# Kernel optimization log

Measured on AMD Instinct MI355X. Metric: run time of the kernel, lower is better.

Reference implementation:

```python
import jax, jax.numpy as jnp
import numpy as np

N_NODES = 100000
N_EDGES = 600000
C_IN, C_HID, C_OUT = 256, 128, 128
LN_EPS = 1e-5
NEG_SLOPE = 0.01  # nn.LeakyReLU default


def setup_inputs() -> dict:
    key = jax.random.key(0)
    ks = jax.random.split(key, 9)
    x = jax.random.normal(ks[0], (N_NODES, C_IN), dtype=jnp.float32)
    x_struct = jax.random.normal(ks[1], (1,), dtype=jnp.float32)  # unused by forward
    x_e = jax.random.normal(ks[2], (1,), dtype=jnp.float32)       # unused by forward
    edge_index = jax.random.randint(ks[3], (2, N_EDGES), 0, N_NODES, dtype=jnp.int64)
    W1 = jax.random.normal(ks[4], (C_IN, C_HID), dtype=jnp.float32) / np.sqrt(C_IN)
    b1 = jnp.zeros((C_HID,), dtype=jnp.float32)
    gamma = jnp.ones((C_HID,), dtype=jnp.float32)
    beta = jnp.zeros((C_HID,), dtype=jnp.float32)
    W2 = jax.random.normal(ks[5], (C_HID, C_OUT), dtype=jnp.float32) / np.sqrt(C_HID)
    b2 = jnp.zeros((C_OUT,), dtype=jnp.float32)
    return {"x": x, "x_struct": x_struct, "x_e": x_e, "edge_index": edge_index,
            "W1": W1, "b1": b1, "gamma": gamma, "beta": beta, "W2": W2, "b2": b2}


def reference(x, x_struct, x_e, edge_index, W1, b1, gamma, beta, W2, b2):
    # dropout is identity in eval mode
    h = jax.nn.leaky_relu(x @ W1 + b1, negative_slope=NEG_SLOPE)  # [N, H]
    # LayerNorm over last dim
    mu = jnp.mean(h, axis=-1, keepdims=True)
    var = jnp.mean(jnp.square(h - mu), axis=-1, keepdims=True)
    h = (h - mu) * jax.lax.rsqrt(var + LN_EPS) * gamma + beta
    # gather source-node features, scatter-min into destination nodes
    src, dst = edge_index[0], edge_index[1]
    msgs = h[src]                                                 # [E, H]
    agg = jax.ops.segment_min(msgs, dst, num_segments=N_NODES)   # empty -> +inf
    counts = jax.ops.segment_sum(jnp.ones((msgs.shape[0],), dtype=jnp.float32),
                                 dst, num_segments=N_NODES)
    agg = jnp.where(counts[:, None] > 0, agg, 0.0)               # PyG fills empty with 0
    return agg @ W2 + b2                                          # [N, C_OUT]
```

## Files before the change

kernel.cpp:

```cpp
#include <hip/hip_runtime.h>
#include <hip/hip_bf16.h>
#include <cstdint>

#define N_NODES 100000
#define N_EDGES 600000
#define C_IN    256
#define C_HID   128
#define C_OUT   128
#define LN_EPS  1e-5f
#define NEG_SLOPE 0.01f

#define NSCAN_BLOCKS 391

typedef float f32x4 __attribute__((ext_vector_type(4)));
typedef __attribute__((ext_vector_type(8))) short frag_ab;

__device__ __forceinline__ void split2(float f, ushort& h, ushort& l) {
    unsigned u = __float_as_uint(f);
    h = (ushort)(u >> 16);
    float d = f - __uint_as_float(u & 0xFFFF0000u);
    l = (ushort)(__float_as_uint(d) >> 16);
}

__device__ __forceinline__ void split8(const float4& p, const float4& q,
                                       frag_ab& hi, frag_ab& lo) {
    ushort h, l;
    split2(p.x, h, l); hi[0] = (short)h; lo[0] = (short)l;
    split2(p.y, h, l); hi[1] = (short)h; lo[1] = (short)l;
    split2(p.z, h, l); hi[2] = (short)h; lo[2] = (short)l;
    split2(p.w, h, l); hi[3] = (short)h; lo[3] = (short)l;
    split2(q.x, h, l); hi[4] = (short)h; lo[4] = (short)l;
    split2(q.y, h, l); hi[5] = (short)h; lo[5] = (short)l;
    split2(q.z, h, l); hi[6] = (short)h; lo[6] = (short)l;
    split2(q.w, h, l); hi[7] = (short)h; lo[7] = (short)l;
}

__device__ __forceinline__ void gload_lds16(const void* g, void* l) {
    __builtin_amdgcn_global_load_lds(
        (const __attribute__((address_space(1))) unsigned int*)g,
        (__attribute__((address_space(3))) unsigned int*)l, 16, 0, 0);
}

__global__ __launch_bounds__(256) void setup_kernel(
    const float* __restrict__ W1, const float* __restrict__ W2,
    ushort* __restrict__ w1s, ushort* __restrict__ w2s, int* __restrict__ dz)
{
    int tg = blockIdx.x * 256 + threadIdx.x;
    if (tg < 2 * N_NODES) dz[tg] = 0;

    const float* W; ushort* out; int t;
    if (tg < 4096)      { W = W1; out = w1s; t = tg; }
    else if (tg < 6144) { W = W2; out = w2s; t = tg - 4096; }
    else return;

    int lane = t & 63;
    int ks   = (t >> 6) & 3;
    int nf   = (t >> 8) & 7;
    int kc   = t >> 11;
    int k0   = kc * 128 + ks * 32 + (lane >> 4) * 8;
    int n    = nf * 16 + (lane & 15);

    frag_ab hi, lo;
    #pragma unroll
    for (int j = 0; j < 8; ++j) {
        ushort h, l;
        split2(W[(size_t)(k0 + j) * 128 + n], h, l);
        hi[j] = (short)h; lo[j] = (short)l;
    }
    size_t fi = ((size_t)(kc * 4 + ks) * 16 + nf * 2) * 64 + lane;
    ((frag_ab*)out)[fi]      = hi;
    ((frag_ab*)out)[fi + 64] = lo;
}

__global__ __launch_bounds__(256) void hist_kernel(const int* __restrict__ ei,
                                                   int* __restrict__ deg) {
    int t = blockIdx.x * 256 + threadIdx.x;
    if (t < N_EDGES) atomicAdd(&deg[ei[N_EDGES + t]], 1);
}

__global__ __launch_bounds__(256) void block_sum_kernel(const int* __restrict__ deg,
                                                        int* __restrict__ bsum) {
    __shared__ int s[256];
    int i = blockIdx.x * 256 + threadIdx.x;
    s[threadIdx.x] = (i < N_NODES) ? deg[i] : 0;
    __syncthreads();
    #pragma unroll
    for (int o = 128; o > 0; o >>= 1) {
        if (threadIdx.x < o) s[threadIdx.x] += s[threadIdx.x + o];
        __syncthreads();
    }
    if (threadIdx.x == 0) bsum[blockIdx.x] = s[0];
}

__global__ __launch_bounds__(512) void scan_bsum_kernel(const int* __restrict__ bsum,
                                                        int* __restrict__ bpre,
                                                        int* __restrict__ offsets) {
    __shared__ int bufA[512], bufB[512];
    int t = threadIdx.x;
    int v = (t < NSCAN_BLOCKS) ? bsum[t] : 0;
    bufA[t] = v;
    __syncthreads();
    int* src = bufA; int* dst = bufB;
    #pragma unroll
    for (int o = 1; o < 512; o <<= 1) {
        dst[t] = src[t] + ((t >= o) ? src[t - o] : 0);
        __syncthreads();
        int* tmp = src; src = dst; dst = tmp;
    }
    if (t < NSCAN_BLOCKS) bpre[t] = src[t] - v;
    if (t == 0) offsets[N_NODES] = N_EDGES;
}

__global__ __launch_bounds__(256) void scan_block_kernel(const int* __restrict__ deg,
                                                         const int* __restrict__ bpre,
                                                         int* __restrict__ offsets) {
    __shared__ int bufA[256], bufB[256];
    int t = threadIdx.x;
    int i = blockIdx.x * 256 + t;
    int v = (i < N_NODES) ? deg[i] : 0;
    bufA[t] = v;
    __syncthreads();
    int* src = bufA; int* dst = bufB;
    #pragma unroll
    for (int o = 1; o < 256; o <<= 1) {
        dst[t] = src[t] + ((t >= o) ? src[t - o] : 0);
        __syncthreads();
        int* tmp = src; src = dst; dst = tmp;
    }
    if (i < N_NODES) offsets[i] = bpre[blockIdx.x] + src[t] - v;
}

__global__ __launch_bounds__(256) void csr_scatter_kernel(const int* __restrict__ ei,
                                                          const int* __restrict__ offsets,
                                                          int* __restrict__ cursor,
                                                          int* __restrict__ csr) {
    int t = blockIdx.x * 256 + threadIdx.x;
    if (t < N_EDGES) {
        int src = ei[t];
        int dst = ei[N_EDGES + t];
        int pos = atomicAdd(&cursor[dst], 1);
        csr[offsets[dst] + pos] = src;
    }
}

__global__ __launch_bounds__(256, 3) void gemm1_ln_mfma_kernel(
    const float* __restrict__ x, const ushort* __restrict__ w1s,
    const float* __restrict__ b1, const float* __restrict__ gamma,
    const float* __restrict__ beta, float* __restrict__ h)
{
    __shared__ ushort sB[2][8192];

    const int tid  = threadIdx.x;
    const int lane = tid & 63;
    const int wv   = tid >> 6;
    const int r16  = lane & 15;
    const int quad = lane >> 4;
    const int row0 = blockIdx.x * 128;

    int rA[2];
    const float* xrow[2];
    #pragma unroll
    for (int mf = 0; mf < 2; ++mf) {
        int r = row0 + wv * 32 + mf * 16 + r16;
        rA[mf] = (r < N_NODES) ? r : (N_NODES - 1);
        xrow[mf] = x + (size_t)rA[mf] * C_IN;
    }

    f32x4 acc[2][8];
    #pragma unroll
    for (int mf = 0; mf < 2; ++mf)
        #pragma unroll
        for (int nf = 0; nf < 8; ++nf)
            acc[mf][nf] = (f32x4){0.f, 0.f, 0.f, 0.f};

    float4 a[2][2][2];

    auto ISSUE = [&](int g) {
        const int par = g & 1;
        const int col0 = (g >> 2) * 128 + (g & 3) * 32 + quad * 8;
        #pragma unroll
        for (int mf = 0; mf < 2; ++mf) {
            const float* xp = xrow[mf] + col0;
            a[par][mf][0] = *(const float4*)(xp);
            a[par][mf][1] = *(const float4*)(xp + 4);
        }
        const char* gsrc = (const char*)w1s + g * 16384 + wv * 4096 + lane * 16;
        char* ldst = (char*)&sB[par][0] + wv * 4096;
        #pragma unroll
        for (int it = 0; it < 4; ++it)
            gload_lds16(gsrc + it * 1024, ldst + it * 1024);
    };

    ISSUE(0);
    #pragma unroll
    for (int g = 0; g < 8; ++g) {
        if (g < 7) {
            ISSUE(g + 1);
            asm volatile("s_waitcnt vmcnt(8)" ::: "memory");
        } else {
            asm volatile("s_waitcnt vmcnt(0)" ::: "memory");
        }
        __builtin_amdgcn_s_barrier();
        __builtin_amdgcn_sched_barrier(0);

        const int par = g & 1;
        frag_ab aHi[2], aLo[2];
        split8(a[par][0][0], a[par][0][1], aHi[0], aLo[0]);
        split8(a[par][1][0], a[par][1][1], aHi[1], aLo[1]);
        const char* bb = (const char*)&sB[par][0] + lane * 16;
        #pragma unroll
        for (int nf = 0; nf < 8; ++nf) {
            frag_ab bHi = *(const frag_ab*)(bb + nf * 2048);
            frag_ab bLo = *(const frag_ab*)(bb + nf * 2048 + 1024);
            acc[0][nf] = __builtin_amdgcn_mfma_f32_16x16x32_bf16(aHi[0], bHi, acc[0][nf], 0, 0, 0);
            acc[0][nf] = __builtin_amdgcn_mfma_f32_16x16x32_bf16(aLo[0], bHi, acc[0][nf], 0, 0, 0);
            acc[0][nf] = __builtin_amdgcn_mfma_f32_16x16x32_bf16(aHi[0], bLo, acc[0][nf], 0, 0, 0);
            acc[1][nf] = __builtin_amdgcn_mfma_f32_16x16x32_bf16(aHi[1], bHi, acc[1][nf], 0, 0, 0);
            acc[1][nf] = __builtin_amdgcn_mfma_f32_16x16x32_bf16(aLo[1], bHi, acc[1][nf], 0, 0, 0);
            acc[1][nf] = __builtin_amdgcn_mfma_f32_16x16x32_bf16(aHi[1], bLo, acc[1][nf], 0, 0, 0);
        }
        __builtin_amdgcn_sched_barrier(0);
        __builtin_amdgcn_s_barrier();
    }

    float b1v[8], gv[8], bv[8];
    #pragma unroll
    for (int nf = 0; nf < 8; ++nf) {
        int cidx = nf * 16 + r16;
        b1v[nf] = b1[cidx]; gv[nf] = gamma[cidx]; bv[nf] = beta[cidx];
    }

    #pragma unroll
    for (int mf = 0; mf < 2; ++mf)
        #pragma unroll
        for (int nf = 0; nf < 8; ++nf)
            #pragma unroll
            for (int rg = 0; rg < 4; ++rg) {
                float v = acc[mf][nf][rg] + b1v[nf];
                acc[mf][nf][rg] = (v > 0.f) ? v : NEG_SLOPE * v;
            }

    #pragma unroll
    for (int mf = 0; mf < 2; ++mf) {
        #pragma unroll
        for (int rg = 0; rg < 4; ++rg) {
            float s = 0.f, ss = 0.f;
            #pragma unroll
            for (int nf = 0; nf < 8; ++nf) {
                float v = acc[mf][nf][rg];
                s += v; ss += v * v;
            }
            #pragma unroll
            for (int m = 1; m < 16; m <<= 1) {
                s  += __shfl_xor(s,  m, 64);
                ss += __shfl_xor(ss, m, 64);
            }
            float mu   = s * (1.f / C_HID);
            float var  = ss * (1.f / C_HID) - mu * mu;
            float rstd = rsqrtf(var + LN_EPS);
            int row = row0 + wv * 32 + mf * 16 + (quad << 2) + rg;
            if (row < N_NODES) {
                #pragma unroll
                for (int nf = 0; nf < 8; ++nf) {
                    float o = (acc[mf][nf][rg] - mu) * rstd * gv[nf] + bv[nf];
                    h[(size_t)row * C_HID + nf * 16 + r16] = o;
                }
            }
        }
    }
}

__global__ __launch_bounds__(256) void gather_min_kernel(
    const float* __restrict__ h, const int* __restrict__ offsets,
    const int* __restrict__ csr, float* __restrict__ agg)
{
    const int lane = threadIdx.x & 63;
    const int row  = blockIdx.x * 4 + (threadIdx.x >> 6);
    if (row >= N_NODES) return;

    const int beg = offsets[row];
    const int end = offsets[row + 1];

    float m0 = INFINITY, m1 = INFINITY;

    for (int j0 = beg; j0 < end; j0 += 64) {
        const int cnt = min(64, end - j0);
        int idx = (lane < cnt) ? csr[j0 + lane] : 0;
        for (int k = 0; k < cnt; k += 4) {
            int s0 = __shfl(idx, k + 0);
            int s1 = __shfl(idx, k + 1);
            int s2 = __shfl(idx, k + 2);
            int s3 = __shfl(idx, k + 3);
            float2 v0 = ((const float2*)(h + (size_t)s0 * C_HID))[lane];
            float2 v1 = make_float2(INFINITY, INFINITY);
            float2 v2 = make_float2(INFINITY, INFINITY);
            float2 v3 = make_float2(INFINITY, INFINITY);
            if (k + 1 < cnt) v1 = ((const float2*)(h + (size_t)s1 * C_HID))[lane];
            if (k + 2 < cnt) v2 = ((const float2*)(h + (size_t)s2 * C_HID))[lane];
            if (k + 3 < cnt) v3 = ((const float2*)(h + (size_t)s3 * C_HID))[lane];
            m0 = fminf(fminf(m0, v0.x), fminf(fminf(v1.x, v2.x), v3.x));
            m1 = fminf(fminf(m1, v0.y), fminf(fminf(v1.y, v2.y), v3.y));
        }
    }

    if (m0 == INFINITY) m0 = 0.f;
    if (m1 == INFINITY) m1 = 0.f;
    ((float2*)(agg + (size_t)row * C_HID))[lane] = make_float2(m0, m1);
}

__global__ __launch_bounds__(256, 3) void gemm2_mfma_kernel(
    const float* __restrict__ agg, const ushort* __restrict__ w2s,
    const float* __restrict__ b2, float* __restrict__ out)
{
    __shared__ ushort sB[2][8192];

    const int tid  = threadIdx.x;
    const int lane = tid & 63;
    const int wv   = tid >> 6;
    const int r16  = lane & 15;
    const int quad = lane >> 4;
    const int row0 = blockIdx.x * 128;

    const float* arow[2];
    #pragma unroll
    for (int mf = 0; mf < 2; ++mf) {
        int r = row0 + wv * 32 + mf * 16 + r16;
        r = (r < N_NODES) ? r : (N_NODES - 1);
        arow[mf] = agg + (size_t)r * C_HID;
    }

    f32x4 acc[2][8];
    #pragma unroll
    for (int mf = 0; mf < 2; ++mf)
        #pragma unroll
        for (int nf = 0; nf < 8; ++nf)
            acc[mf][nf] = (f32x4){0.f, 0.f, 0.f, 0.f};

    float4 a[2][2][2];

    auto ISSUE = [&](int g) {
        const int par = g & 1;
        const int col0 = g * 32 + quad * 8;
        #pragma unroll
        for (int mf = 0; mf < 2; ++mf) {
            const float* ap = arow[mf] + col0;
            a[par][mf][0] = *(const float4*)(ap);
            a[par][mf][1] = *(const float4*)(ap + 4);
        }
        const char* gsrc = (const char*)w2s + g * 16384 + wv * 4096 + lane * 16;
        char* ldst = (char*)&sB[par][0] + wv * 4096;
        #pragma unroll
        for (int it = 0; it < 4; ++it)
            gload_lds16(gsrc + it * 1024, ldst + it * 1024);
    };

    ISSUE(0);
    #pragma unroll
    for (int g = 0; g < 4; ++g) {
        if (g < 3) {
            ISSUE(g + 1);
            asm volatile("s_waitcnt vmcnt(8)" ::: "memory");
        } else {
            asm volatile("s_waitcnt vmcnt(0)" ::: "memory");
        }
        __builtin_amdgcn_s_barrier();
        __builtin_amdgcn_sched_barrier(0);

        const int par = g & 1;
        frag_ab aHi[2], aLo[2];
        split8(a[par][0][0], a[par][0][1], aHi[0], aLo[0]);
        split8(a[par][1][0], a[par][1][1], aHi[1], aLo[1]);
        const char* bb = (const char*)&sB[par][0] + lane * 16;
        #pragma unroll
        for (int nf = 0; nf < 8; ++nf) {
            frag_ab bHi = *(const frag_ab*)(bb + nf * 2048);
            frag_ab bLo = *(const frag_ab*)(bb + nf * 2048 + 1024);
            acc[0][nf] = __builtin_amdgcn_mfma_f32_16x16x32_bf16(aHi[0], bHi, acc[0][nf], 0, 0, 0);
            acc[0][nf] = __builtin_amdgcn_mfma_f32_16x16x32_bf16(aLo[0], bHi, acc[0][nf], 0, 0, 0);
            acc[0][nf] = __builtin_amdgcn_mfma_f32_16x16x32_bf16(aHi[0], bLo, acc[0][nf], 0, 0, 0);
            acc[1][nf] = __builtin_amdgcn_mfma_f32_16x16x32_bf16(aHi[1], bHi, acc[1][nf], 0, 0, 0);
            acc[1][nf] = __builtin_amdgcn_mfma_f32_16x16x32_bf16(aLo[1], bHi, acc[1][nf], 0, 0, 0);
            acc[1][nf] = __builtin_amdgcn_mfma_f32_16x16x32_bf16(aHi[1], bLo, acc[1][nf], 0, 0, 0);
        }
        __builtin_amdgcn_sched_barrier(0);
        __builtin_amdgcn_s_barrier();
    }

    float b2v[8];
    #pragma unroll
    for (int nf = 0; nf < 8; ++nf) b2v[nf] = b2[nf * 16 + r16];

    #pragma unroll
    for (int mf = 0; mf < 2; ++mf) {
        #pragma unroll
        for (int rg = 0; rg < 4; ++rg) {
            int row = row0 + wv * 32 + mf * 16 + (quad << 2) + rg;
            if (row < N_NODES) {
                #pragma unroll
                for (int nf = 0; nf < 8; ++nf)
                    out[(size_t)row * C_OUT + nf * 16 + r16] = acc[mf][nf][rg] + b2v[nf];
            }
        }
    }
}

extern "C" void kernel_launch(void* const* d_in, const int* in_sizes, int n_in,
                              void* d_out, int out_size, void* d_ws, size_t ws_size,
                              hipStream_t stream)
{
    const float* x     = (const float*)d_in[0];
    const int*   ei    = (const int*)d_in[3];
    const float* W1    = (const float*)d_in[4];
    const float* b1    = (const float*)d_in[5];
    const float* gamma = (const float*)d_in[6];
    const float* beta  = (const float*)d_in[7];
    const float* W2    = (const float*)d_in[8];
    const float* b2    = (const float*)d_in[9];
    float*       out   = (float*)d_out;

    char* p = (char*)d_ws;
    float*  h       = (float*)p;           p += (size_t)N_NODES * C_HID * 4;
    float*  agg     = (float*)p;           p += (size_t)N_NODES * C_HID * 4;
    int*    deg     = (int*)p;             p += 400000;
    int*    cursor  = (int*)p;             p += 400000;
    int*    offsets = (int*)p;             p += 400016;
    int*    bsum    = (int*)p;             p += 1600;
    int*    bpre    = (int*)p;             p += 1600;
    int*    csr     = (int*)p;             p += (size_t)N_EDGES * 4;
    ushort* w1s     = (ushort*)p;          p += 131072;
    ushort* w2s     = (ushort*)p;

    const int grid_e    = (N_EDGES + 255) / 256;
    const int grid_gemm = (N_NODES + 127) / 128;

    setup_kernel<<<grid_gemm, 256, 0, stream>>>(W1, W2, w1s, w2s, deg);
    hist_kernel<<<grid_e, 256, 0, stream>>>(ei, deg);
    block_sum_kernel<<<NSCAN_BLOCKS, 256, 0, stream>>>(deg, bsum);
    scan_bsum_kernel<<<1, 512, 0, stream>>>(bsum, bpre, offsets);
    scan_block_kernel<<<NSCAN_BLOCKS, 256, 0, stream>>>(deg, bpre, offsets);
    csr_scatter_kernel<<<grid_e, 256, 0, stream>>>(ei, offsets, cursor, csr);
    gemm1_ln_mfma_kernel<<<grid_gemm, 256, 0, stream>>>(x, w1s, b1, gamma, beta, h);
    gather_min_kernel<<<(N_NODES + 3) / 4, 256, 0, stream>>>(h, offsets, csr, agg);
    gemm2_mfma_kernel<<<grid_gemm, 256, 0, stream>>>(agg, w2s, b2, out);
}
```

Baseline: 342.3 us.

## Deepen GEMM load pipelines to four stages and batch gather loads by eight

Both MFMA GEMM kernels move from double-buffered to four-stage buffering of the A registers and the LDS B tiles, keeping three groups of global loads in flight with adjusted vmcnt waits. Launch bounds drop from 3 to 2 blocks per SM to make room for the larger LDS and register footprint. The gather-min kernel now issues eight independent row loads per step instead of four, raising memory-level parallelism. The cost is lower occupancy in the GEMMs, which may offset the latency-hiding gains.

```diff
diff --git a/kernel.cpp b/kernel.cpp
--- a/kernel.cpp
+++ b/kernel.cpp
@@ -14,6 +14,8 @@
 
 typedef float f32x4 __attribute__((ext_vector_type(4)));
 typedef __attribute__((ext_vector_type(8))) short frag_ab;
+
+#define WAITV(N) asm volatile("s_waitcnt vmcnt(" #N ")" ::: "memory")
 
 __device__ __forceinline__ void split2(float f, ushort& h, ushort& l) {
     unsigned u = __float_as_uint(f);
@@ -143,12 +145,12 @@
     }
 }
 
-__global__ __launch_bounds__(256, 3) void gemm1_ln_mfma_kernel(
+__global__ __launch_bounds__(256, 2) void gemm1_ln_mfma_kernel(
     const float* __restrict__ x, const ushort* __restrict__ w1s,
     const float* __restrict__ b1, const float* __restrict__ gamma,
     const float* __restrict__ beta, float* __restrict__ h)
 {
-    __shared__ ushort sB[2][8192];
+    __shared__ ushort sB[4][8192];
 
     const int tid  = threadIdx.x;
     const int lane = tid & 63;
@@ -157,13 +159,12 @@
     const int quad = lane >> 4;
     const int row0 = blockIdx.x * 128;
 
-    int rA[2];
     const float* xrow[2];
     #pragma unroll
     for (int mf = 0; mf < 2; ++mf) {
         int r = row0 + wv * 32 + mf * 16 + r16;
-        rA[mf] = (r < N_NODES) ? r : (N_NODES - 1);
-        xrow[mf] = x + (size_t)rA[mf] * C_IN;
+        r = (r < N_NODES) ? r : (N_NODES - 1);
+        xrow[mf] = x + (size_t)r * C_IN;
     }
 
     f32x4 acc[2][8];
@@ -173,10 +174,10 @@
         for (int nf = 0; nf < 8; ++nf)
             acc[mf][nf] = (f32x4){0.f, 0.f, 0.f, 0.f};
 
-    float4 a[2][2][2];
+    float4 a[4][2][2];
 
     auto ISSUE = [&](int g) {
-        const int par = g & 1;
+        const int par = g & 3;
         const int col0 = (g >> 2) * 128 + (g & 3) * 32 + quad * 8;
         #pragma unroll
         for (int mf = 0; mf < 2; ++mf) {
@@ -191,19 +192,17 @@
             gload_lds16(gsrc + it * 1024, ldst + it * 1024);
     };
 
-    ISSUE(0);
+    ISSUE(0); ISSUE(1); ISSUE(2);
     #pragma unroll
     for (int g = 0; g < 8; ++g) {
-        if (g < 7) {
-            ISSUE(g + 1);
-            asm volatile("s_waitcnt vmcnt(8)" ::: "memory");
-        } else {
-            asm volatile("s_waitcnt vmcnt(0)" ::: "memory");
-        }
+        if (g < 5) { ISSUE(g + 3); WAITV(24); }
+        else if (g == 5) WAITV(16);
+        else if (g == 6) WAITV(8);
+        else             WAITV(0);
         __builtin_amdgcn_s_barrier();
         __builtin_amdgcn_sched_barrier(0);
 
-        const int par = g & 1;
+        const int par = g & 3;
         frag_ab aHi[2], aLo[2];
         split8(a[par][0][0], a[par][0][1], aHi[0], aLo[0]);
         split8(a[par][1][0], a[par][1][1], aHi[1], aLo[1]);
@@ -286,20 +285,22 @@
     for (int j0 = beg; j0 < end; j0 += 64) {
         const int cnt = min(64, end - j0);
         int idx = (lane < cnt) ? csr[j0 + lane] : 0;
-        for (int k = 0; k < cnt; k += 4) {
-            int s0 = __shfl(idx, k + 0);
-            int s1 = __shfl(idx, k + 1);
-            int s2 = __shfl(idx, k + 2);
-            int s3 = __shfl(idx, k + 3);
-            float2 v0 = ((const float2*)(h + (size_t)s0 * C_HID))[lane];
-            float2 v1 = make_float2(INFINITY, INFINITY);
-            float2 v2 = make_float2(INFINITY, INFINITY);
-            float2 v3 = make_float2(INFINITY, INFINITY);
-            if (k + 1 < cnt) v1 = ((const float2*)(h + (size_t)s1 * C_HID))[lane];
-            if (k + 2 < cnt) v2 = ((const float2*)(h + (size_t)s2 * C_HID))[lane];
-            if (k + 3 < cnt) v3 = ((const float2*)(h + (size_t)s3 * C_HID))[lane];
-            m0 = fminf(fminf(m0, v0.x), fminf(fminf(v1.x, v2.x), v3.x));
-            m1 = fminf(fminf(m1, v0.y), fminf(fminf(v1.y, v2.y), v3.y));
+        for (int k = 0; k < cnt; k += 8) {
+            float2 v[8];
+            #pragma unroll
+            for (int i = 0; i < 8; ++i) {
+                int kk = k + i;
+                int s = __shfl(idx, (kk < cnt) ? kk : 0);
+                if (kk < cnt)
+                    v[i] = ((const float2*)(h + (size_t)s * C_HID))[lane];
+                else
+                    v[i] = make_float2(INFINITY, INFINITY);
+            }
+            #pragma unroll
+            for (int i = 0; i < 8; ++i) {
+                m0 = fminf(m0, v[i].x);
+                m1 = fminf(m1, v[i].y);
+            }
         }
     }
 
@@ -308,11 +309,11 @@
     ((float2*)(agg + (size_t)row * C_HID))[lane] = make_float2(m0, m1);
 }
 
-__global__ __launch_bounds__(256, 3) void gemm2_mfma_kernel(
+__global__ __launch_bounds__(256, 2) void gemm2_mfma_kernel(
     const float* __restrict__ agg, const ushort* __restrict__ w2s,
     const float* __restrict__ b2, float* __restrict__ out)
 {
-    __shared__ ushort sB[2][8192];
+    __shared__ ushort sB[4][8192];
 
     const int tid  = threadIdx.x;
     const int lane = tid & 63;
@@ -336,10 +337,10 @@
         for (int nf = 0; nf < 8; ++nf)
             acc[mf][nf] = (f32x4){0.f, 0.f, 0.f, 0.f};
 
-    float4 a[2][2][2];
+    float4 a[4][2][2];
 
     auto ISSUE = [&](int g) {
-        const int par = g & 1;
+        const int par = g & 3;
         const int col0 = g * 32 + quad * 8;
         #pragma unroll
         for (int mf = 0; mf < 2; ++mf) {
@@ -354,19 +355,17 @@
             gload_lds16(gsrc + it * 1024, ldst + it * 1024);
     };
 
-    ISSUE(0);
+    ISSUE(0); ISSUE(1); ISSUE(2);
     #pragma unroll
     for (int g = 0; g < 4; ++g) {
-        if (g < 3) {
-            ISSUE(g + 1);
-            asm volatile("s_waitcnt vmcnt(8)" ::: "memory");
-        } else {
-            asm volatile("s_waitcnt vmcnt(0)" ::: "memory");
-        }
+        if (g == 0) { ISSUE(3); WAITV(24); }
+        else if (g == 1) WAITV(16);
+        else if (g == 2) WAITV(8);
+        else             WAITV(0);
         __builtin_amdgcn_s_barrier();
         __builtin_amdgcn_sched_barrier(0);
 
-        const int par = g & 1;
+        const int par = g & 3;
         frag_ab aHi[2], aLo[2];
         split8(a[par][0][0], a[par][0][1], aHi[0], aLo[0]);
         split8(a[par][1][0], a[par][1][1], aHi[1], aLo[1]);
```

After: 335.6 us. No clear change (-2.0%).
